# Performance work log

Measured on AMD Instinct MI355X. Metric: run time of the kernel, lower is better.

The kernel has to match this reference:

```python
import jax, jax.numpy as jnp
import numpy as np

EPS = 1e-06  # used both as eps and as the F.threshold threshold (mqjs passes eps as th)


def _pair_log_dist_sum(x1, x2, th):
    # dist[i,j] = ||x1_i||^2 + ||x2_j||^2 - 2 x1_i . x2_j  (n x n)
    x1x2 = x1 @ x2.T
    sq1 = jnp.sum(x1 * x1, axis=1)[:, None]
    sq2 = jnp.sum(x2 * x2, axis=1)[None, :]
    dist = sq1 + sq2 - 2.0 * x1x2
    # F.threshold(dist, th, 1): values <= th -> 1; then clamp(min=1), sqrt, log, row-sum
    dist = jnp.where(dist > th, dist, 1.0)
    dist = jnp.maximum(dist, 1.0)
    return jnp.sum(0.5 * jnp.log(dist), axis=1)  # log(sqrt(d)) == 0.5*log(d)


def _mqjs(inp, tgt, eps):
    n = inp.shape[0]
    x1 = inp.reshape(n, -1)
    x2 = tgt.reshape(n, -1)
    p = (x1 + x2) / 2.0
    ce = _pair_log_dist_sum(x1, p, eps) + _pair_log_dist_sum(x2, p, eps)
    se = _pair_log_dist_sum(x1, x1, eps) * (n / (n - 1))
    return jnp.mean(ce - se)


def setup_inputs() -> dict:
    key = jax.random.key(0)
    k1, k2 = jax.random.split(key)
    n, d = 8192, 256
    inp = jax.random.normal(k1, (n, d), dtype=jnp.float32)
    tgt = jax.random.normal(k2, (n, d), dtype=jnp.float32)
    return {"input": inp, "target": tgt}


def reference(input, target):
    return _mqjs(input, target, EPS)
```

## Files before the change

### kernel.cpp

```cpp
#include <hip/hip_runtime.h>

#define N 8192
#define D 256
#define BM 128
#define BJ 64
#define JG 8
#define GJ (N / BJ / JG)
#define GI (N / BM)
#define NPART (3 * GI * GJ)

typedef int   i32x4 __attribute__((ext_vector_type(4)));
typedef int   i32x8 __attribute__((ext_vector_type(8)));
typedef float f32x4 __attribute__((ext_vector_type(4)));
typedef float f32x2 __attribute__((ext_vector_type(2)));

__device__ __forceinline__ unsigned pack_fp8x4(float a, float b, float c, float d) {
    unsigned lo = __builtin_amdgcn_cvt_pk_fp8_f32(a, b, 0, false);
    return __builtin_amdgcn_cvt_pk_fp8_f32(c, d, lo, true);
}
__device__ __forceinline__ float dequant_sumsq(unsigned q) {
    const float v0 = __builtin_amdgcn_cvt_f32_fp8(q, 0);
    const float v1 = __builtin_amdgcn_cvt_f32_fp8(q, 1);
    const float v2 = __builtin_amdgcn_cvt_f32_fp8(q, 2);
    const float v3 = __builtin_amdgcn_cvt_f32_fp8(q, 3);
    return fmaf(v0, v0, fmaf(v1, v1, fmaf(v2, v2, v3 * v3)));
}

__global__ void prep_kernel(const float* __restrict__ x1, const float* __restrict__ x2,
                            unsigned* __restrict__ x1q, unsigned* __restrict__ x2q,
                            unsigned* __restrict__ pq,
                            float* __restrict__ sq1, float* __restrict__ sq2,
                            float* __restrict__ sqp) {
    const int tid = threadIdx.x, lane = tid & 63, wv = tid >> 6;
    const int row = blockIdx.x * 4 + wv;
    const size_t eb = (size_t)row * D + lane * 4;
    const float4 a = *(const float4*)(x1 + eb);
    const float4 b = *(const float4*)(x2 + eb);
    const float px = 0.5f * (a.x + b.x), py = 0.5f * (a.y + b.y);
    const float pz = 0.5f * (a.z + b.z), pw = 0.5f * (a.w + b.w);
    const unsigned qa = pack_fp8x4(a.x, a.y, a.z, a.w);
    const unsigned qb = pack_fp8x4(b.x, b.y, b.z, b.w);
    const unsigned qp = pack_fp8x4(px, py, pz, pw);
    const size_t wb = (size_t)row * (D / 4) + lane;
    x1q[wb] = qa; x2q[wb] = qb; pq[wb] = qp;
    float s1 = dequant_sumsq(qa), s2 = dequant_sumsq(qb), sp = dequant_sumsq(qp);
    #pragma unroll
    for (int o = 32; o > 0; o >>= 1) {
        s1 += __shfl_down(s1, o, 64);
        s2 += __shfl_down(s2, o, 64);
        sp += __shfl_down(sp, o, 64);
    }
    if (lane == 0) { sq1[row] = s1; sq2[row] = s2; sqp[row] = sp; }
}

__device__ __forceinline__ f32x4 mfma8(i32x8 a, i32x8 b, f32x4 c) {
    return __builtin_amdgcn_mfma_scale_f32_16x16x128_f8f6f4(
        a, b, c, 0, 0, 0, 0x7F7F7F7F, 0, 0x7F7F7F7F);
}

__device__ __forceinline__ i32x8 read_frag(const unsigned char* Ts, int m, int quad) {
    const int r7 = m & 7;
    const i32x4 lo = *(const i32x4*)(Ts + m * 128 + ((((2 * quad)     ^ r7)) << 4));
    const i32x4 hi = *(const i32x4*)(Ts + m * 128 + ((((2 * quad + 1) ^ r7)) << 4));
    i32x8 f;
    f[0] = lo[0]; f[1] = lo[1]; f[2] = lo[2]; f[3] = lo[3];
    f[4] = hi[0]; f[5] = hi[1]; f[6] = hi[2]; f[7] = hi[3];
    return f;
}

__device__ __forceinline__ void stageB(const unsigned char* __restrict__ g,
                                       unsigned char* s, int rowbase, size_t kb,
                                       int wv, int srow, int sblk) {
    #pragma unroll
    for (int it = 0; it < 2; ++it) {
        const int grp = wv * 2 + it;
        const int row = grp * 8 + srow;
        __builtin_amdgcn_global_load_lds(
            (const __attribute__((address_space(1))) void*)(g + (size_t)(rowbase + row) * D + kb + sblk * 16),
            (__attribute__((address_space(3))) void*)(s + grp * 1024), 16, 0, 0);
    }
}

__device__ __forceinline__ float logsumP(const f32x4 (&acc)[4][2],
                                         const f32x2 (&sa01)[4], const f32x2 (&sa23)[4],
                                         const float sb[2]) {
    float s = 0.0f;
    #pragma unroll
    for (int ti = 0; ti < 4; ++ti) {
        f32x2 pr = {1.0f, 1.0f};
        #pragma unroll
        for (int tj = 0; tj < 2; ++tj) {
            const f32x2 sbv = {sb[tj], sb[tj]};
            const f32x2 t01 = sa01[ti] + sbv, t23 = sa23[ti] + sbv;
            const f32x2 v01 = {acc[ti][tj][0], acc[ti][tj][1]};
            const f32x2 v23 = {acc[ti][tj][2], acc[ti][tj][3]};
            f32x2 d01 = t01 - 2.0f * v01;
            f32x2 d23 = t23 - 2.0f * v23;
            d01 = __builtin_elementwise_max(d01, (f32x2){1.0f, 1.0f});
            d23 = __builtin_elementwise_max(d23, (f32x2){1.0f, 1.0f});
            pr *= d01; pr *= d23;
        }
        s += __log2f(pr.x * pr.y);
    }
    return s;
}

__device__ __forceinline__ float logsumStraddle(const f32x4 (&acc)[4][2],
                                                const f32x2 (&sa01)[4], const f32x2 (&sa23)[4],
                                                const float sb[2],
                                                int wr, int wc, int quad, int l15,
                                                int I0, int J0) {
    float s = 0.0f;
    #pragma unroll
    for (int ti = 0; ti < 4; ++ti) {
        #pragma unroll
        for (int tj = 0; tj < 2; ++tj) {
            const int j = J0 + wc * 32 + tj * 16 + l15;
            float pr = 1.0f;
            #pragma unroll
            for (int r = 0; r < 4; ++r) {
                const int i = I0 + wr * 64 + ti * 16 + quad * 4 + r;
                const float sav = (r < 2) ? ((r & 1) ? sa01[ti].y : sa01[ti].x)
                                          : ((r & 1) ? sa23[ti].y : sa23[ti].x);
                float d = fmaf(-2.0f, acc[ti][tj][r], sav + sb[tj]);
                d = fmaxf(d, 1.0f);
                const float t = (j > i) ? d : 1.0f;
                const float u = (j >= i) ? d : 1.0f;
                pr *= t * u;
            }
            s += __log2f(pr);
        }
    }
    return s;
}

__global__ __launch_bounds__(256) void mqjs_main(
    const unsigned char* __restrict__ x1q, const unsigned char* __restrict__ x2q,
    const unsigned char* __restrict__ pq,
    const float* __restrict__ sq1, const float* __restrict__ sq2,
    const float* __restrict__ sqp, float* __restrict__ partials) {

    __shared__ __align__(16) unsigned char Bs[3][2 * BJ * 128];
    __shared__ float red[4];

    const int tid = threadIdx.x;
    const int lane = tid & 63;
    const int wv = tid >> 6;
    const int wr = wv >> 1, wc = wv & 1;
    const int quad = lane >> 4, l15 = lane & 15;
    const int srow = lane >> 3;
    const int sblk = (lane & 7) ^ srow;

    const int z = blockIdx.z;
    const int I0 = blockIdx.y * BM;
    const int jbase = blockIdx.x * JG;
    const int pid = (z * GI + blockIdx.y) * GJ + blockIdx.x;
    const float wse = -(float)N / (float)(N - 1);

    int jj0 = 0;
    if (z == 2) {
        jj0 = 2 * (int)blockIdx.y - jbase;
        if (jj0 < 0) jj0 = 0;
        if (jj0 >= JG) { if (tid == 0) partials[pid] = 0.0f; return; }
    }

    const unsigned char* Ag = (z == 1) ? x2q : x1q;
    const unsigned char* Bg = (z == 2) ? x1q : pq;
    const float* sqAg = (z == 1) ? sq2 : sq1;
    const float* sqBg = (z == 2) ? sq1 : sqp;

    i32x8 af[2][4];
    f32x2 sa01[4], sa23[4];
    #pragma unroll
    for (int ti = 0; ti < 4; ++ti) {
        #pragma unroll
        for (int kc = 0; kc < 2; ++kc) {
            const size_t ro = (size_t)(I0 + wr * 64 + ti * 16 + l15) * D + kc * 128 + quad * 32;
            af[kc][ti] = *(const i32x8*)(Ag + ro);
        }
        const int sbase = I0 + wr * 64 + ti * 16 + quad * 4;
        sa01[ti] = (f32x2){sqAg[sbase], sqAg[sbase + 1]};
        sa23[ti] = (f32x2){sqAg[sbase + 2], sqAg[sbase + 3]};
    }

    stageB(Bg, Bs[0],        (jbase + jj0) * BJ, 0,   wv, srow, sblk);
    stageB(Bg, Bs[0] + 8192, (jbase + jj0) * BJ, 128, wv, srow, sblk);
    if (jj0 + 1 < JG) {
        stageB(Bg, Bs[1],        (jbase + jj0 + 1) * BJ, 0,   wv, srow, sblk);
        stageB(Bg, Bs[1] + 8192, (jbase + jj0 + 1) * BJ, 128, wv, srow, sblk);
    }

    float tsum = 0.0f;
    const f32x4 zero4 = {0.0f, 0.0f, 0.0f, 0.0f};
    int cur = 0;

    for (int jj = jj0; jj < JG; ++jj) {
        const int J0 = (jbase + jj) * BJ;

        if (jj + 1 < JG) asm volatile("s_waitcnt vmcnt(4)" ::: "memory");
        else             asm volatile("s_waitcnt vmcnt(0)" ::: "memory");
        asm volatile("s_barrier" ::: "memory");

        float sb[2];
        #pragma unroll
        for (int tj = 0; tj < 2; ++tj) sb[tj] = sqBg[J0 + wc * 32 + tj * 16 + l15];

        if (jj + 2 < JG) {
            const int b2 = (cur == 0) ? 2 : cur - 1;
            stageB(Bg, Bs[b2],        (jbase + jj + 2) * BJ, 0,   wv, srow, sblk);
            stageB(Bg, Bs[b2] + 8192, (jbase + jj + 2) * BJ, 128, wv, srow, sblk);
        }

        i32x8 bfr0[2], bfr1[2];
        #pragma unroll
        for (int tj = 0; tj < 2; ++tj) {
            bfr0[tj] = read_frag(Bs[cur],        wc * 32 + tj * 16 + l15, quad);
            bfr1[tj] = read_frag(Bs[cur] + 8192, wc * 32 + tj * 16 + l15, quad);
        }

        f32x4 acc[4][2];
        __builtin_amdgcn_s_setprio(1);
        #pragma unroll
        for (int ti = 0; ti < 4; ++ti)
            #pragma unroll
            for (int tj = 0; tj < 2; ++tj)
                acc[ti][tj] = mfma8(af[0][ti], bfr0[tj], zero4);
        #pragma unroll
        for (int ti = 0; ti < 4; ++ti)
            #pragma unroll
            for (int tj = 0; tj < 2; ++tj)
                acc[ti][tj] = mfma8(af[1][ti], bfr1[tj], acc[ti][tj]);
        __builtin_amdgcn_s_setprio(0);

        if (z < 2) {
            tsum += 0.5f * logsumP(acc, sa01, sa23, sb);
        } else if (J0 >= I0 + BM) {
            tsum += wse * logsumP(acc, sa01, sa23, sb);
        } else {
            tsum += 0.5f * wse * logsumStraddle(acc, sa01, sa23, sb, wr, wc, quad, l15, I0, J0);
        }

        cur = (cur == 2) ? 0 : cur + 1;
    }

    tsum *= 0.6931471805599453f;
    #pragma unroll
    for (int o = 32; o > 0; o >>= 1) tsum += __shfl_down(tsum, o, 64);
    if (lane == 0) red[wv] = tsum;
    __syncthreads();
    if (tid == 0) partials[pid] = red[0] + red[1] + red[2] + red[3];
}

__global__ void finalize_kernel(const float* __restrict__ partials, float* __restrict__ out) {
    const int tid = threadIdx.x;
    const float4 v = ((const float4*)partials)[tid];
    double s = (double)v.x + (double)v.y + (double)v.z + (double)v.w;
    #pragma unroll
    for (int o = 32; o > 0; o >>= 1) s += __shfl_down(s, o, 64);
    __shared__ double r[12];
    if ((tid & 63) == 0) r[tid >> 6] = s;
    __syncthreads();
    if (tid == 0) {
        double t = 0.0;
        #pragma unroll
        for (int i = 0; i < 12; ++i) t += r[i];
        out[0] = (float)(t / (double)N);
    }
}

extern "C" void kernel_launch(void* const* d_in, const int* in_sizes, int n_in,
                              void* d_out, int out_size, void* d_ws, size_t ws_size,
                              hipStream_t stream) {
    const float* x1 = (const float*)d_in[0];
    const float* x2 = (const float*)d_in[1];

    char* ws = (char*)d_ws;
    const size_t MBYTES = (size_t)N * D;
    unsigned* x1q = (unsigned*)(ws);
    unsigned* x2q = (unsigned*)(ws + MBYTES);
    unsigned* pq  = (unsigned*)(ws + 2 * MBYTES);
    float* sq1 = (float*)(ws + 3 * MBYTES);
    float* sq2 = (float*)(ws + 3 * MBYTES + (size_t)N * 4);
    float* sqp = (float*)(ws + 3 * MBYTES + (size_t)N * 8);
    float* partials = (float*)(ws + 3 * MBYTES + (size_t)N * 12);

    prep_kernel<<<N / 4, 256, 0, stream>>>(x1, x2, x1q, x2q, pq, sq1, sq2, sqp);
    mqjs_main<<<dim3(GJ, GI, 3), 256, 0, stream>>>(
        (const unsigned char*)x1q, (const unsigned char*)x2q, (const unsigned char*)pq,
        sq1, sq2, sqp, partials);
    finalize_kernel<<<1, 768, 0, stream>>>(partials, (float*)d_out);
}
```

Before: 147.0 us.

## Software-pipeline MFMA tiles with the previous tile's log epilogue

Restructures the j-tile loop so each iteration issues the MFMA work for tile jj, then runs the log-sum epilogue for tile jj-1, using ping-pong accumulator sets. The aim is to overlap the matrix-core latency with the VALU/transcendental epilogue instead of serializing them. It also drops the s_setprio hints and computes the buffer index with a modulo. In exchange it doubles the accumulator registers, which could lower occupancy or cause spills.

```diff
diff --git a/kernel.cpp b/kernel.cpp
--- a/kernel.cpp
+++ b/kernel.cpp
@@ -192,56 +192,64 @@
 
     float tsum = 0.0f;
     const f32x4 zero4 = {0.0f, 0.0f, 0.0f, 0.0f};
-    int cur = 0;
-
-    for (int jj = jj0; jj < JG; ++jj) {
-        const int J0 = (jbase + jj) * BJ;
-
+
+    auto MFMA_TILE = [&](int jj, f32x4 (&accC)[4][2], float (&sbC)[2]) {
         if (jj + 1 < JG) asm volatile("s_waitcnt vmcnt(4)" ::: "memory");
         else             asm volatile("s_waitcnt vmcnt(0)" ::: "memory");
         asm volatile("s_barrier" ::: "memory");
-
-        float sb[2];
-        #pragma unroll
-        for (int tj = 0; tj < 2; ++tj) sb[tj] = sqBg[J0 + wc * 32 + tj * 16 + l15];
-
+        const int J0 = (jbase + jj) * BJ;
+        sbC[0] = sqBg[J0 + wc * 32 + l15];
+        sbC[1] = sqBg[J0 + wc * 32 + 16 + l15];
         if (jj + 2 < JG) {
-            const int b2 = (cur == 0) ? 2 : cur - 1;
+            const int b2 = (jj + 2 - jj0) % 3;
             stageB(Bg, Bs[b2],        (jbase + jj + 2) * BJ, 0,   wv, srow, sblk);
             stageB(Bg, Bs[b2] + 8192, (jbase + jj + 2) * BJ, 128, wv, srow, sblk);
         }
-
+        const int cur = (jj - jj0) % 3;
         i32x8 bfr0[2], bfr1[2];
         #pragma unroll
         for (int tj = 0; tj < 2; ++tj) {
             bfr0[tj] = read_frag(Bs[cur],        wc * 32 + tj * 16 + l15, quad);
             bfr1[tj] = read_frag(Bs[cur] + 8192, wc * 32 + tj * 16 + l15, quad);
         }
-
-        f32x4 acc[4][2];
-        __builtin_amdgcn_s_setprio(1);
         #pragma unroll
         for (int ti = 0; ti < 4; ++ti)
             #pragma unroll
             for (int tj = 0; tj < 2; ++tj)
-                acc[ti][tj] = mfma8(af[0][ti], bfr0[tj], zero4);
+                accC[ti][tj] = mfma8(af[0][ti], bfr0[tj], zero4);
         #pragma unroll
         for (int ti = 0; ti < 4; ++ti)
             #pragma unroll
             for (int tj = 0; tj < 2; ++tj)
-                acc[ti][tj] = mfma8(af[1][ti], bfr1[tj], acc[ti][tj]);
-        __builtin_amdgcn_s_setprio(0);
-
+                accC[ti][tj] = mfma8(af[1][ti], bfr1[tj], accC[ti][tj]);
+    };
+
+    auto EPI = [&](int jjPrev, const f32x4 (&accP)[4][2], const float (&sbP)[2]) {
+        const int J0p = (jbase + jjPrev) * BJ;
         if (z < 2) {
-            tsum += 0.5f * logsumP(acc, sa01, sa23, sb);
-        } else if (J0 >= I0 + BM) {
-            tsum += wse * logsumP(acc, sa01, sa23, sb);
+            tsum += 0.5f * logsumP(accP, sa01, sa23, sbP);
+        } else if (J0p >= I0 + BM) {
+            tsum += wse * logsumP(accP, sa01, sa23, sbP);
         } else {
-            tsum += 0.5f * wse * logsumStraddle(acc, sa01, sa23, sb, wr, wc, quad, l15, I0, J0);
-        }
-
-        cur = (cur == 2) ? 0 : cur + 1;
-    }
+            tsum += 0.5f * wse * logsumStraddle(accP, sa01, sa23, sbP, wr, wc, quad, l15, I0, J0p);
+        }
+    };
+
+    f32x4 accA[4][2], accB[4][2];
+    float sbA[2], sbB[2];
+
+    MFMA_TILE(jj0, accA, sbA);
+    for (int jj = jj0 + 1; jj < JG; ++jj) {
+        if (((jj - jj0) & 1) == 1) {
+            MFMA_TILE(jj, accB, sbB);
+            EPI(jj - 1, accA, sbA);
+        } else {
+            MFMA_TILE(jj, accA, sbA);
+            EPI(jj - 1, accB, sbB);
+        }
+    }
+    if (((JG - jj0) & 1) == 1) EPI(JG - 1, accA, sbA);
+    else                       EPI(JG - 1, accB, sbB);
 
     tsum *= 0.6931471805599453f;
     #pragma unroll
```

Result: slower. 191.7 us (+30.4%).

## Split block tile across eight waves with 32-row A strips per wave

Applied to the files above, without the earlier changes.

Doubles the block from 256 to 512 threads, so each of the eight waves owns a 32x32 output sub-tile instead of 64x32. Per-wave A fragments and accumulators are halved, and B staging is spread over more waves, each issuing one load per half. The aim is to lower register pressure and raise wave occupancy so LDS/global latency and the log epilogue overlap better. In exchange, B fragments are read from LDS by twice as many waves per tile, and the vmcnt wait counts were adjusted to match the new load count.

```diff
diff --git a/kernel.cpp b/kernel.cpp
--- a/kernel.cpp
+++ b/kernel.cpp
@@ -68,25 +68,21 @@
     return f;
 }
 
-__device__ __forceinline__ void stageB(const unsigned char* __restrict__ g,
-                                       unsigned char* s, int rowbase, size_t kb,
-                                       int wv, int srow, int sblk) {
-    #pragma unroll
-    for (int it = 0; it < 2; ++it) {
-        const int grp = wv * 2 + it;
-        const int row = grp * 8 + srow;
-        __builtin_amdgcn_global_load_lds(
-            (const __attribute__((address_space(1))) void*)(g + (size_t)(rowbase + row) * D + kb + sblk * 16),
-            (__attribute__((address_space(3))) void*)(s + grp * 1024), 16, 0, 0);
-    }
-}
-
-__device__ __forceinline__ float logsumP(const f32x4 (&acc)[4][2],
-                                         const f32x2 (&sa01)[4], const f32x2 (&sa23)[4],
+__device__ __forceinline__ void stageB8(const unsigned char* __restrict__ g,
+                                        unsigned char* s, int rowbase, size_t kb,
+                                        int wv, int srow, int sblk) {
+    const int row = wv * 8 + srow;
+    __builtin_amdgcn_global_load_lds(
+        (const __attribute__((address_space(1))) void*)(g + (size_t)(rowbase + row) * D + kb + sblk * 16),
+        (__attribute__((address_space(3))) void*)(s + wv * 1024), 16, 0, 0);
+}
+
+__device__ __forceinline__ float logsumP(const f32x4 (&acc)[2][2],
+                                         const f32x2 (&sa01)[2], const f32x2 (&sa23)[2],
                                          const float sb[2]) {
     float s = 0.0f;
     #pragma unroll
-    for (int ti = 0; ti < 4; ++ti) {
+    for (int ti = 0; ti < 2; ++ti) {
         f32x2 pr = {1.0f, 1.0f};
         #pragma unroll
         for (int tj = 0; tj < 2; ++tj) {
@@ -105,21 +101,21 @@
     return s;
 }
 
-__device__ __forceinline__ float logsumStraddle(const f32x4 (&acc)[4][2],
-                                                const f32x2 (&sa01)[4], const f32x2 (&sa23)[4],
+__device__ __forceinline__ float logsumStraddle(const f32x4 (&acc)[2][2],
+                                                const f32x2 (&sa01)[2], const f32x2 (&sa23)[2],
                                                 const float sb[2],
                                                 int wr, int wc, int quad, int l15,
                                                 int I0, int J0) {
     float s = 0.0f;
     #pragma unroll
-    for (int ti = 0; ti < 4; ++ti) {
+    for (int ti = 0; ti < 2; ++ti) {
         #pragma unroll
         for (int tj = 0; tj < 2; ++tj) {
             const int j = J0 + wc * 32 + tj * 16 + l15;
             float pr = 1.0f;
             #pragma unroll
             for (int r = 0; r < 4; ++r) {
-                const int i = I0 + wr * 64 + ti * 16 + quad * 4 + r;
+                const int i = I0 + wr * 32 + ti * 16 + quad * 4 + r;
                 const float sav = (r < 2) ? ((r & 1) ? sa01[ti].y : sa01[ti].x)
                                           : ((r & 1) ? sa23[ti].y : sa23[ti].x);
                 float d = fmaf(-2.0f, acc[ti][tj][r], sav + sb[tj]);
@@ -134,14 +130,14 @@
     return s;
 }
 
-__global__ __launch_bounds__(256) void mqjs_main(
+__global__ __launch_bounds__(512, 4) void mqjs_main(
     const unsigned char* __restrict__ x1q, const unsigned char* __restrict__ x2q,
     const unsigned char* __restrict__ pq,
     const float* __restrict__ sq1, const float* __restrict__ sq2,
     const float* __restrict__ sqp, float* __restrict__ partials) {
 
     __shared__ __align__(16) unsigned char Bs[3][2 * BJ * 128];
-    __shared__ float red[4];
+    __shared__ float red[8];
 
     const int tid = threadIdx.x;
     const int lane = tid & 63;
@@ -169,25 +165,26 @@
     const float* sqAg = (z == 1) ? sq2 : sq1;
     const float* sqBg = (z == 2) ? sq1 : sqp;
 
-    i32x8 af[2][4];
-    f32x2 sa01[4], sa23[4];
-    #pragma unroll
-    for (int ti = 0; ti < 4; ++ti) {
+    i32x8 af[2][2];
+    f32x2 sa01[2], sa23[2];
+    #pragma unroll
+    for (int ti = 0; ti < 2; ++ti) {
         #pragma unroll
         for (int kc = 0; kc < 2; ++kc) {
-            const size_t ro = (size_t)(I0 + wr * 64 + ti * 16 + l15) * D + kc * 128 + quad * 32;
+            const size_t ro = (size_t)(I0 + wr * 32 + ti * 16 + l15) * D + kc * 128 + quad * 32;
             af[kc][ti] = *(const i32x8*)(Ag + ro);
         }
-        const int sbase = I0 + wr * 64 + ti * 16 + quad * 4;
-        sa01[ti] = (f32x2){sqAg[sbase], sqAg[sbase + 1]};
-        sa23[ti] = (f32x2){sqAg[sbase + 2], sqAg[sbase + 3]};
-    }
-
-    stageB(Bg, Bs[0],        (jbase + jj0) * BJ, 0,   wv, srow, sblk);
-    stageB(Bg, Bs[0] + 8192, (jbase + jj0) * BJ, 128, wv, srow, sblk);
+        const int sbase = I0 + wr * 32 + ti * 16 + quad * 4;
+        const float4 sv = *(const float4*)(sqAg + sbase);
+        sa01[ti] = (f32x2){sv.x, sv.y};
+        sa23[ti] = (f32x2){sv.z, sv.w};
+    }
+
+    stageB8(Bg, Bs[0],        (jbase + jj0) * BJ, 0,   wv, srow, sblk);
+    stageB8(Bg, Bs[0] + 8192, (jbase + jj0) * BJ, 128, wv, srow, sblk);
     if (jj0 + 1 < JG) {
-        stageB(Bg, Bs[1],        (jbase + jj0 + 1) * BJ, 0,   wv, srow, sblk);
-        stageB(Bg, Bs[1] + 8192, (jbase + jj0 + 1) * BJ, 128, wv, srow, sblk);
+        stageB8(Bg, Bs[1],        (jbase + jj0 + 1) * BJ, 0,   wv, srow, sblk);
+        stageB8(Bg, Bs[1] + 8192, (jbase + jj0 + 1) * BJ, 128, wv, srow, sblk);
     }
 
     float tsum = 0.0f;
@@ -197,18 +194,18 @@
     for (int jj = jj0; jj < JG; ++jj) {
         const int J0 = (jbase + jj) * BJ;
 
-        if (jj + 1 < JG) asm volatile("s_waitcnt vmcnt(4)" ::: "memory");
+        if (jj + 1 < JG) asm volatile("s_waitcnt vmcnt(2)" ::: "memory");
         else             asm volatile("s_waitcnt vmcnt(0)" ::: "memory");
         asm volatile("s_barrier" ::: "memory");
 
         float sb[2];
-        #pragma unroll
-        for (int tj = 0; tj < 2; ++tj) sb[tj] = sqBg[J0 + wc * 32 + tj * 16 + l15];
+        sb[0] = sqBg[J0 + wc * 32 + l15];
+        sb[1] = sqBg[J0 + wc * 32 + 16 + l15];
 
         if (jj + 2 < JG) {
             const int b2 = (cur == 0) ? 2 : cur - 1;
-            stageB(Bg, Bs[b2],        (jbase + jj + 2) * BJ, 0,   wv, srow, sblk);
-            stageB(Bg, Bs[b2] + 8192, (jbase + jj + 2) * BJ, 128, wv, srow, sblk);
+            stageB8(Bg, Bs[b2],        (jbase + jj + 2) * BJ, 0,   wv, srow, sblk);
+            stageB8(Bg, Bs[b2] + 8192, (jbase + jj + 2) * BJ, 128, wv, srow, sblk);
         }
 
         i32x8 bfr0[2], bfr1[2];
@@ -218,15 +215,15 @@
             bfr1[tj] = read_frag(Bs[cur] + 8192, wc * 32 + tj * 16 + l15, quad);
         }
 
-        f32x4 acc[4][2];
+        f32x4 acc[2][2];
         __builtin_amdgcn_s_setprio(1);
         #pragma unroll
-        for (int ti = 0; ti < 4; ++ti)
+        for (int ti = 0; ti < 2; ++ti)
             #pragma unroll
             for (int tj = 0; tj < 2; ++tj)
                 acc[ti][tj] = mfma8(af[0][ti], bfr0[tj], zero4);
         #pragma unroll
-        for (int ti = 0; ti < 4; ++ti)
+        for (int ti = 0; ti < 2; ++ti)
             #pragma unroll
             for (int tj = 0; tj < 2; ++tj)
                 acc[ti][tj] = mfma8(af[1][ti], bfr1[tj], acc[ti][tj]);
@@ -248,7 +245,12 @@
     for (int o = 32; o > 0; o >>= 1) tsum += __shfl_down(tsum, o, 64);
     if (lane == 0) red[wv] = tsum;
     __syncthreads();
-    if (tid == 0) partials[pid] = red[0] + red[1] + red[2] + red[3];
+    if (tid == 0) {
+        float t = 0.0f;
+        #pragma unroll
+        for (int i = 0; i < 8; ++i) t += red[i];
+        partials[pid] = t;
+    }
 }
 
 __global__ void finalize_kernel(const float* __restrict__ partials, float* __restrict__ out) {
@@ -285,7 +287,7 @@
     float* partials = (float*)(ws + 3 * MBYTES + (size_t)N * 12);
 
     prep_kernel<<<N / 4, 256, 0, stream>>>(x1, x2, x1q, x2q, pq, sq1, sq2, sqp);
-    mqjs_main<<<dim3(GJ, GI, 3), 256, 0, stream>>>(
+    mqjs_main<<<dim3(GJ, GI, 3), 512, 0, stream>>>(
         (const unsigned char*)x1q, (const unsigned char*)x2q, (const unsigned char*)pq,
         sq1, sq2, sqp, partials);
     finalize_kernel<<<1, 768, 0, stream>>>(partials, (float*)d_out);
```

Result: faster. 139.5 us (-5.1%).
